# Optimization experiments

Measured on AMD Instinct MI355X. Metric: run time of the kernel, lower is better.

## Reference

```python
import jax, jax.numpy as jnp
import numpy as np

B, NG, F, ED, EG = 1024, 32, 16, 6, 256
H1, C1, C2 = 5, 80, 160
OBS, ACT = 512, 2
NT, ET = B * NG, B * EG
LOG_STD_MIN, LOG_STD_MAX = -5.0, 2.0


def setup_inputs():
    key = jax.random.key(0)
    ks = jax.random.split(key, 32)
    def rn(i, shape, s=0.05):
        return (jax.random.normal(ks[i], shape) * s).astype(jnp.float32)
    # within-graph random edges, then offset per graph (PyG Batch layout)
    off = (jnp.arange(B) * NG)[None, :, None]
    edge_index = (jax.random.randint(ks[0], (2, B, EG), 0, NG) + off).reshape(2, ET).astype(jnp.int32)
    return {
        "x": jax.random.normal(ks[1], (NT, F), dtype=jnp.float32),
        "edge_index": edge_index,
        "edge_attr": jax.random.normal(ks[2], (ET, ED), dtype=jnp.float32),
        "Wl1": rn(3, (H1 * C1, F)), "bl1": rn(4, (H1 * C1,)),
        "Wr1": rn(5, (H1 * C1, F)), "br1": rn(6, (H1 * C1,)),
        "We1": rn(7, (H1 * C1, ED)), "att1": rn(8, (H1, C1)), "bc1": rn(9, (H1 * C1,)),
        "Wl2": rn(10, (C2, H1 * C1)), "bl2": rn(11, (C2,)),
        "Wr2": rn(12, (C2, H1 * C1)), "br2": rn(13, (C2,)),
        "We2": rn(14, (C2, ED)), "att2": rn(15, (1, C2)), "bc2": rn(16, (C2,)),
        "Wd1": rn(17, (NG, C2)), "bd1": rn(18, (NG,)),
        "Wd2": rn(19, (OBS, NG)), "bd2": rn(20, (OBS,)),
        "Wf1": rn(21, (256, OBS)), "bf1": rn(22, (256,)),
        "Wf2": rn(23, (256, 256)), "bf2": rn(24, (256,)),
        "Wm": rn(25, (ACT, 256)), "bm": rn(26, (ACT,)),
        "Ws": rn(27, (ACT, 256)), "bs": rn(28, (ACT,)),
    }


def gatv2(x, src, dst, edge_attr, Wl, bl, Wr, br, We, att, bias, H, C):
    """PyG GATv2Conv (concat heads, no self loops, negative_slope=0.2, eval mode)."""
    N = x.shape[0]; E = src.shape[0]
    xl = x @ Wl.T + bl              # [N, H*C] source transform (also the message)
    xr = x @ Wr.T + br              # [N, H*C] target transform
    e = edge_attr @ We.T            # [E, H*C]
    msg = xl[src].reshape(E, H, C)
    pre = msg + xr[dst].reshape(E, H, C) + e.reshape(E, H, C)
    score = jnp.sum(jax.nn.leaky_relu(pre, 0.2) * att, axis=-1)  # [E, H]
    # segment softmax over incoming edges of each destination node
    mx = jax.ops.segment_max(score, dst, num_segments=N)
    ex = jnp.exp(score - mx[dst])
    den = jax.ops.segment_sum(ex, dst, num_segments=N)
    alpha = ex / (den[dst] + 1e-16)
    out = jax.ops.segment_sum(alpha[..., None] * msg, dst, num_segments=N)
    return out.reshape(N, H * C) + bias


def reference(x, edge_index, edge_attr, Wl1, bl1, Wr1, br1, We1, att1, bc1,
              Wl2, bl2, Wr2, br2, We2, att2, bc2, Wd1, bd1, Wd2, bd2,
              Wf1, bf1, Wf2, bf2, Wm, bm, Ws, bs):
    src, dst = edge_index[0], edge_index[1]
    h = jax.nn.relu(gatv2(x, src, dst, edge_attr, Wl1, bl1, Wr1, br1, We1, att1, bc1, H1, C1))
    h = jax.nn.relu(gatv2(h, src, dst, edge_attr, Wl2, bl2, Wr2, br2, We2, att2, bc2, 1, C2))
    ego = h[jnp.arange(B) * NG]                      # first node of each graph, [B, C2]
    d = jnp.tanh((ego @ Wd1.T + bd1) @ Wd2.T + bd2)  # dense head -> [B, OBS]
    h1 = jax.nn.relu(d @ Wf1.T + bf1)
    h2 = jax.nn.relu(h1 @ Wf2.T + bf2)
    mean = h2 @ Wm.T + bm
    log_std = LOG_STD_MIN + 0.5 * (LOG_STD_MAX - LOG_STD_MIN) * (jnp.tanh(h2 @ Ws.T + bs) + 1.0)
    return mean, log_std
```

## Files before the change

### kernel.cpp

```cpp
#include <hip/hip_runtime.h>

#define B_    1024
#define NG_   32
#define F_    16
#define ED_   6
#define EG_   256
#define ET_   262144
#define H1_   5
#define C1_   80
#define HC1_  400
#define C2_   160
#define OBS_  512

#define S1_   408
#define SG_   400
#define CAP_  40960

typedef unsigned short ushort8v __attribute__((ext_vector_type(8)));

__device__ __forceinline__ float bf2f(unsigned short u) {
  return __uint_as_float(((unsigned int)u) << 16);
}
__device__ __forceinline__ unsigned short f2bf(float f) {
  unsigned int u = __float_as_uint(f);
  u = u + 0x7FFFu + ((u >> 16) & 1u);
  return (unsigned short)(u >> 16);
}
__device__ __forceinline__ float dot8(ushort8v hv, float4 wa, float4 wb, float acc) {
  acc = fmaf(bf2f(hv[0]), wa.x, acc);
  acc = fmaf(bf2f(hv[1]), wa.y, acc);
  acc = fmaf(bf2f(hv[2]), wa.z, acc);
  acc = fmaf(bf2f(hv[3]), wa.w, acc);
  acc = fmaf(bf2f(hv[4]), wb.x, acc);
  acc = fmaf(bf2f(hv[5]), wb.y, acc);
  acc = fmaf(bf2f(hv[6]), wb.z, acc);
  acc = fmaf(bf2f(hv[7]), wb.w, acc);
  return acc;
}

__global__ __launch_bounds__(512, 2)
void k1_transform_bucket(
    const float* __restrict__ x, const int* __restrict__ eidx,
    const float* __restrict__ Wl1, const float* __restrict__ bl1,
    const float* __restrict__ Wr1, const float* __restrict__ br1,
    unsigned short* __restrict__ xlg, unsigned short* __restrict__ xrg,
    int* __restrict__ eorder_g, int* __restrict__ bstart_g)
{
  __shared__ __align__(16) unsigned short xlL[NG_ * S1_];
  __shared__ __align__(16) unsigned short xrL[NG_ * S1_];
  __shared__ float xloc[NG_ * F_];
  __shared__ int   edst[EG_];
  const int b = blockIdx.x, tid = threadIdx.x;
  const int n0 = b * NG_, eb = b * EG_;

  if (tid < EG_) edst[tid] = eidx[ET_ + eb + tid] - n0;
  xloc[tid] = x[n0 * F_ + tid];
  __syncthreads();

  if (tid < 448) {
    for (int t = 0; t < 2; ++t) {
      const int ch = tid + t * 448;
      if (ch >= 800) break;
      const bool isL = (ch < 400);
      const int  c   = isL ? ch : ch - 400;
      const float* Wp = (isL ? Wl1 : Wr1) + c * F_;
      const float bias = isL ? bl1[c] : br1[c];
      unsigned short* dst = (isL ? xlL : xrL) + c;
      float w[16];
#pragma unroll
      for (int qk = 0; qk < 4; ++qk) {
        float4 v = *(const float4*)(Wp + qk * 4);
        w[qk*4+0] = v.x; w[qk*4+1] = v.y; w[qk*4+2] = v.z; w[qk*4+3] = v.w;
      }
      for (int n = 0; n < NG_; n += 2) {
        const float* xa = &xloc[n * F_];
        float accA = bias, accB = bias;
#pragma unroll
        for (int qk = 0; qk < 4; ++qk) {
          float4 a  = *(const float4*)(xa + qk * 4);
          float4 bv = *(const float4*)(xa + F_ + qk * 4);
          accA = fmaf(a.x,  w[qk*4+0], accA); accA = fmaf(a.y,  w[qk*4+1], accA);
          accA = fmaf(a.z,  w[qk*4+2], accA); accA = fmaf(a.w,  w[qk*4+3], accA);
          accB = fmaf(bv.x, w[qk*4+0], accB); accB = fmaf(bv.y, w[qk*4+1], accB);
          accB = fmaf(bv.z, w[qk*4+2], accB); accB = fmaf(bv.w, w[qk*4+3], accB);
        }
        dst[n * S1_]       = f2bf(accA);
        dst[(n + 1) * S1_] = f2bf(accB);
      }
    }
  } else {
    const int lane = tid & 63;
    const int d    = lane & 31;
    const int half = lane >> 5;
    int cnt = 0;
    const int4* ed4 = (const int4*)edst;
    for (int i = 0; i < 32; ++i) {
      int4 v = ed4[half * 32 + i];
      cnt += (v.x == d) + (v.y == d) + (v.z == d) + (v.w == d);
    }
    const int cnt_lo = __shfl(cnt, d);
    const int total  = cnt + __shfl_xor(cnt, 32);
    int pre = total;
#pragma unroll
    for (int off = 1; off < 32; off <<= 1) {
      int tt = __shfl(pre, lane - off);
      if (d >= off) pre += tt;
    }
    const int start = pre - total;
    if (lane < 32) {
      bstart_g[b * 33 + d] = start;
      if (d == 31) bstart_g[b * 33 + 32] = pre;
    }
    int p = start + (half ? cnt_lo : 0);
    for (int i = 0; i < 32; ++i) {
      int4 v = ed4[half * 32 + i];
      const int e = half * 128 + i * 4;
      if (v.x == d) eorder_g[eb + p++] = e;
      if (v.y == d) eorder_g[eb + p++] = e + 1;
      if (v.z == d) eorder_g[eb + p++] = e + 2;
      if (v.w == d) eorder_g[eb + p++] = e + 3;
    }
  }
  __syncthreads();

  for (int i = tid; i < 3200; i += 512) {
    const bool isR = (i >= 1600);
    const int idx = isR ? i - 1600 : i;
    const int n = idx / 50, c8 = idx - n * 50;
    const ushort8v v = *(const ushort8v*)&(isR ? xrL : xlL)[n * S1_ + c8 * 8];
    *(ushort8v*)&(isR ? xrg : xlg)[(n0 + n) * SG_ + c8 * 8] = v;
  }
}

__global__ __launch_bounds__(1024, 1)
void k0b_pack(const int* __restrict__ bstart_g, const int* __restrict__ eorder_g,
              const int* __restrict__ eidx,
              int* __restrict__ egoOff, int* __restrict__ meta_node,
              int* __restrict__ meta_eid)
{
  __shared__ int scanBuf[B_];
  const int b = threadIdx.x;
  const int nE = bstart_g[b * 33 + 1];
  scanBuf[b] = nE;
  __syncthreads();
  for (int off = 1; off < B_; off <<= 1) {
    int v = (b >= off) ? scanBuf[b - off] : 0;
    __syncthreads();
    scanBuf[b] += v;
    __syncthreads();
  }
  const int start = scanBuf[b] - nE;
  egoOff[b] = start;
  if (b == B_ - 1) egoOff[B_] = scanBuf[b];
  if (start + nE <= CAP_) {
    for (int j = 0; j < nE; ++j) {
      const int e = eorder_g[b * EG_ + j];
      meta_node[start + j] = eidx[b * EG_ + e];
      meta_eid[start + j]  = b * EG_ + e;
    }
  }
}

__global__ __launch_bounds__(512, 2)
void k2_scores_aggregate(
    const unsigned short* __restrict__ xlg, const unsigned short* __restrict__ xrg,
    const int* __restrict__ eidx, const float* __restrict__ eattr,
    const float* __restrict__ We1, const float* __restrict__ att1,
    const float* __restrict__ bc1,
    const int* __restrict__ eorder_g, const int* __restrict__ bstart_g,
    unsigned short* __restrict__ hg)
{
  __shared__ __align__(16) unsigned short xl[NG_ * S1_];
  __shared__ __align__(16) unsigned short xr[NG_ * S1_];
  __shared__ float sc0[EG_ * H1_];
  __shared__ float sc1[EG_ * H1_];
  __shared__ float ea[EG_ * ED_];
  __shared__ int   esrc[EG_], edst[EG_], eorder[EG_];
  __shared__ int   bstart[NG_ + 1];
  __shared__ float deninv[NG_ * H1_];

  const int b = blockIdx.x, tid = threadIdx.x;
  const int n0 = b * NG_, eb = b * EG_;

  for (int i = tid; i < 3200; i += 512) {
    const bool isR = (i >= 1600);
    const int idx = isR ? i - 1600 : i;
    const int n = idx / 50, c8 = idx - n * 50;
    const ushort8v v = *(const ushort8v*)&(isR ? xrg : xlg)[(n0 + n) * SG_ + c8 * 8];
    *(ushort8v*)&(isR ? xr : xl)[n * S1_ + c8 * 8] = v;
  }
  if (tid < EG_) {
    esrc[tid]   = eidx[eb + tid] - n0;
    edst[tid]   = eidx[ET_ + eb + tid] - n0;
    eorder[tid] = eorder_g[eb + tid];
  }
  for (int i = tid; i < EG_ * ED_; i += 512) ea[i] = eattr[eb * ED_ + i];
  if (tid < NG_ + 1) bstart[tid] = bstart_g[b * 33 + tid];
  __syncthreads();

  {
    const int e = tid & 255;
    const int s = __builtin_amdgcn_readfirstlane((int)(tid >> 8) & 1);
    float* const scp = s ? sc1 : sc0;
    const int sl = esrc[e], dl = edst[e];
    const float e0 = ea[e*ED_+0], e1 = ea[e*ED_+1], e2 = ea[e*ED_+2];
    const float e3 = ea[e*ED_+3], e4 = ea[e*ED_+4], e5 = ea[e*ED_+5];
    const unsigned short* xlrow = &xl[sl * S1_ + s * 40];
    const unsigned short* xrrow = &xr[dl * S1_ + s * 40];
#pragma unroll
    for (int h = 0; h < H1_; ++h) {
      float sh = 0.f;
#pragma unroll
      for (int co = 0; co < 5; ++co) {
        const int coff  = h * C1_ + co * 8;
        const int cbase = coff + s * 40;
        ushort8v av = *(const ushort8v*)(xlrow + coff);
        ushort8v rv = *(const ushort8v*)(xrrow + coff);
#pragma unroll
        for (int u = 0; u < 8; ++u) {
          const float* wv6 = &We1[(cbase + u) * ED_];
          float t0 = fmaf(wv6[1], e1, wv6[0] * e0);
          float t1 = fmaf(wv6[3], e3, wv6[2] * e2);
          float t2 = fmaf(wv6[5], e5, wv6[4] * e4);
          float p = (bf2f(av[u]) + bf2f(rv[u])) + (t0 + (t1 + t2));
          p = fmaxf(p, 0.2f * p);
          sh = fmaf(p, att1[cbase + u], sh);
        }
      }
      scp[e * H1_ + h] = sh;
    }
  }
  __syncthreads();

  if (tid < NG_ * H1_) {
    const int d = tid & 31, h = tid >> 5;
    const int s0 = bstart[d], s1 = bstart[d + 1];
    float m = -INFINITY;
    for (int k = s0; k < s1; ++k) {
      const int e5i = eorder[k] * H1_ + h;
      m = fmaxf(m, sc0[e5i] + sc1[e5i]);
    }
    float den = 0.f;
    for (int k = s0; k < s1; ++k) {
      const int e5i = eorder[k] * H1_ + h;
      float t = expf(sc0[e5i] + sc1[e5i] - m);
      den += t;
      sc0[e5i] = t;
    }
    deninv[tid] = 1.f / (den + 1e-16f);
  }
  __syncthreads();

  for (int idx = tid; idx < NG_ * 50; idx += 512) {
    const int d  = idx / 50;
    const int co = idx - d * 50;
    const int c  = co * 8;
    const int h  = co / 10;
    const int s0 = bstart[d], s1 = bstart[d + 1];
    float acc[8] = {0.f,0.f,0.f,0.f,0.f,0.f,0.f,0.f};
    for (int k = s0; k < s1; ++k) {
      const int e = eorder[k];
      const float al = sc0[e * H1_ + h];
      ushort8v xv = *(const ushort8v*)(&xl[esrc[e] * S1_ + c]);
#pragma unroll
      for (int u = 0; u < 8; ++u) acc[u] = fmaf(al, bf2f(xv[u]), acc[u]);
    }
    const float inv = deninv[h * 32 + d];
    ushort8v hv;
#pragma unroll
    for (int u = 0; u < 8; ++u)
      hv[u] = f2bf(fmaxf(fmaf(acc[u], inv, bc1[c + u]), 0.f));
    *(ushort8v*)&hg[(n0 + d) * SG_ + c] = hv;
  }
}

__global__ __launch_bounds__(512, 2)
void k3a_gemm(const unsigned short* __restrict__ hg,
              const int* __restrict__ meta_node, const int* __restrict__ egoOff,
              const float* __restrict__ Wl2, const float* __restrict__ bl2,
              const float* __restrict__ Wr2, const float* __restrict__ br2,
              float* __restrict__ msgP, float* __restrict__ xr2v_g)
{
  __shared__ __align__(16) unsigned short rows[64 * S1_];
  __shared__ int rnode[64];
  __shared__ int sTot;
  const int tid = threadIdx.x;
  const bool isX = (blockIdx.x < 16);
  if (tid == 0) sTot = egoOff[B_];
  __syncthreads();
  const int total = sTot;

  const float* W    = isX ? Wr2 : Wl2;
  const float* bias = isX ? br2 : bl2;
  float* outB       = isX ? xr2v_g : msgP;

  const int es = tid & 15;
  const int cg = tid >> 4;
  const float* wp[5];
#pragma unroll
  for (int i = 0; i < 5; ++i) wp[i] = &W[(size_t)(cg * 5 + i) * HC1_];

  int c = isX ? (int)blockIdx.x : (int)blockIdx.x - 16;
  const int cstep = (int)gridDim.x - 16;

  for (;;) {
    const int r0 = c * 64;
    int nr;
    if (isX) nr = 64;
    else { if (r0 >= total) break; nr = min(64, total - r0); }

    __syncthreads();
    if (tid < 64) rnode[tid] = (tid < nr) ? (isX ? (r0 + tid) * NG_ : meta_node[r0 + tid]) : 0;
    __syncthreads();
    for (int i = tid; i < 64 * 50; i += 512) {
      const int r = i / 50, o8 = i - r * 50;
      if (r < nr)
        *(ushort8v*)&rows[r * S1_ + o8 * 8] =
            *(const ushort8v*)&hg[(size_t)rnode[r] * SG_ + o8 * 8];
    }
    __syncthreads();

    float acc[4][5] = {};
#pragma unroll 2
    for (int ko = 0; ko < 50; ++ko) {
      const int k = ko * 8;
      ushort8v rv[4];
#pragma unroll
      for (int t = 0; t < 4; ++t)
        rv[t] = *(const ushort8v*)&rows[(es + 16 * t) * S1_ + k];
#pragma unroll
      for (int i = 0; i < 5; ++i) {
        const float4 wa = *(const float4*)(wp[i] + k);
        const float4 wb = *(const float4*)(wp[i] + k + 4);
#pragma unroll
        for (int t = 0; t < 4; ++t)
          acc[t][i] = dot8(rv[t], wa, wb, acc[t][i]);
      }
    }

#pragma unroll
    for (int t = 0; t < 4; ++t) {
      const int r = es + 16 * t;
      if (r < nr) {
        float* op = outB + (size_t)(r0 + r) * C2_ + cg * 5;
#pragma unroll
        for (int i = 0; i < 5; ++i) op[i] = acc[t][i] + bias[cg * 5 + i];
      }
    }
    if (isX) break;
    c += cstep;
  }
}

__global__ __launch_bounds__(64, 4)
void k3b_finish(const float* __restrict__ eattr,
                const float* __restrict__ We2, const float* __restrict__ att2,
                const float* __restrict__ bc2,
                const int* __restrict__ egoOff, const int* __restrict__ meta_eid,
                const float* __restrict__ msgP, const float* __restrict__ xr2v_g,
                float* __restrict__ egoH)
{
  __shared__ float xr2s[C2_];
  __shared__ float scq[EG_], wq[EG_];
  const int b = blockIdx.x, ln = threadIdx.x;
  const int off = egoOff[b];
  const int nE  = egoOff[b + 1] - off;

  if (ln < 40) *(float4*)&xr2s[ln * 4] = *(const float4*)&xr2v_g[(size_t)b * C2_ + ln * 4];

  const int s = ln >> 3, q8 = ln & 7;
  for (int base = 0; base < nE; base += 8) {
    const int j = base + s;
    float sv = 0.f;
    if (j < nE) {
      const int eid = meta_eid[off + j];
      const float* ap = &eattr[(size_t)eid * ED_];
      const float f0 = ap[0], f1 = ap[1], f2 = ap[2];
      const float f3 = ap[3], f4 = ap[4], f5 = ap[5];
      const float* mrow = &msgP[(size_t)(off + j) * C2_];
      for (int i = 0; i < 20; ++i) {
        const int c2 = q8 * 20 + i;
        const float* wv6 = &We2[c2 * ED_];
        float t0 = fmaf(wv6[1], f1, wv6[0] * f0);
        float t1 = fmaf(wv6[3], f3, wv6[2] * f2);
        float t2 = fmaf(wv6[5], f5, wv6[4] * f4);
        float pp = mrow[c2] + xr2s[c2] + (t0 + (t1 + t2));
        pp = fmaxf(pp, 0.2f * pp);
        sv = fmaf(pp, att2[c2], sv);
      }
    }
    sv += __shfl_xor(sv, 1); sv += __shfl_xor(sv, 2); sv += __shfl_xor(sv, 4);
    if (q8 == 0 && j < nE) scq[j] = sv;
  }

  float m = -INFINITY;
  for (int j = ln; j < nE; j += 64) m = fmaxf(m, scq[j]);
#pragma unroll
  for (int d = 1; d < 64; d <<= 1) m = fmaxf(m, __shfl_xor(m, d));

  float den = 0.f;
  for (int j = ln; j < nE; j += 64) {
    const float w = expf(scq[j] - m);
    wq[j] = w;
    den += w;
  }
#pragma unroll
  for (int d = 1; d < 64; d <<= 1) den += __shfl_xor(den, d);
  const float inv = 1.f / (den + 1e-16f);

  float o0 = 0.f, o1 = 0.f, o2 = 0.f;
  for (int j = 0; j < nE; ++j) {
    const float w = wq[j];
    const float* mrow = &msgP[(size_t)(off + j) * C2_];
    o0 = fmaf(w, mrow[ln], o0);
    o1 = fmaf(w, mrow[ln + 64], o1);
    if (ln + 128 < C2_) o2 = fmaf(w, mrow[ln + 128], o2);
  }
  egoH[(size_t)b * C2_ + ln]      = fmaxf(fmaf(o0, inv, bc2[ln]), 0.f);
  egoH[(size_t)b * C2_ + ln + 64] = fmaxf(fmaf(o1, inv, bc2[ln + 64]), 0.f);
  if (ln + 128 < C2_)
    egoH[(size_t)b * C2_ + ln + 128] = fmaxf(fmaf(o2, inv, bc2[ln + 128]), 0.f);
}

__global__ __launch_bounds__(512, 2)
void mlp_head_kernel(
    const float* __restrict__ egoH,
    const float* __restrict__ Wd1, const float* __restrict__ bd1,
    const float* __restrict__ Wd2, const float* __restrict__ bd2,
    const float* __restrict__ Wf1, const float* __restrict__ bf1,
    const float* __restrict__ Wf2, const float* __restrict__ bf2,
    const float* __restrict__ Wm,  const float* __restrict__ bm,
    const float* __restrict__ Ws,  const float* __restrict__ bs,
    float* __restrict__ out)
{
  __shared__ float hE[4 * C2_];
  __shared__ float t1[4 * NG_];
  __shared__ float dbuf[4 * OBS_];
  __shared__ float f1b[4 * 256];
  __shared__ float f2b[4 * 256];

  const int g0  = blockIdx.x * 4;
  const int tid = threadIdx.x;

  for (int i = tid; i < 4 * C2_; i += 512) hE[i] = egoH[g0 * C2_ + i];
  __syncthreads();

  if (tid < 4 * NG_) {
    const int g = tid >> 5, o = tid & 31;
    float acc = bd1[o];
    const float* w  = &Wd1[o * C2_];
    const float* hp = &hE[g * C2_];
    for (int k = 0; k < C2_; k += 4) {
      float4 hv = *(const float4*)(hp + k);
      float4 wv = *(const float4*)(w + k);
      acc = fmaf(hv.x, wv.x, acc); acc = fmaf(hv.y, wv.y, acc);
      acc = fmaf(hv.z, wv.z, acc); acc = fmaf(hv.w, wv.w, acc);
    }
    t1[tid] = acc;
  }
  __syncthreads();

  for (int idx = tid; idx < 4 * OBS_; idx += 512) {
    const int g = idx >> 9, o = idx & 511;
    float acc = bd2[o];
    const float* w  = &Wd2[o * NG_];
    const float* tp = &t1[g * NG_];
#pragma unroll
    for (int k = 0; k < NG_; k += 4) {
      float4 tv = *(const float4*)(tp + k);
      float4 wv = *(const float4*)(w + k);
      acc = fmaf(tv.x, wv.x, acc); acc = fmaf(tv.y, wv.y, acc);
      acc = fmaf(tv.z, wv.z, acc); acc = fmaf(tv.w, wv.w, acc);
    }
    dbuf[idx] = tanhf(acc);
  }
  __syncthreads();

  {
    const int o = tid & 255, gg = tid >> 8;
    const float* w  = &Wf1[o * OBS_];
    const float* dA = &dbuf[(gg * 2 + 0) * OBS_];
    const float* dB = &dbuf[(gg * 2 + 1) * OBS_];
    float a0 = bf1[o], a1 = a0;
#pragma unroll 2
    for (int k = 0; k < OBS_; k += 4) {
      float4 wv = *(const float4*)(w + k);
      float4 xA = *(const float4*)(dA + k);
      float4 xB = *(const float4*)(dB + k);
      a0 = fmaf(xA.x, wv.x, a0); a0 = fmaf(xA.y, wv.y, a0);
      a0 = fmaf(xA.z, wv.z, a0); a0 = fmaf(xA.w, wv.w, a0);
      a1 = fmaf(xB.x, wv.x, a1); a1 = fmaf(xB.y, wv.y, a1);
      a1 = fmaf(xB.z, wv.z, a1); a1 = fmaf(xB.w, wv.w, a1);
    }
    f1b[(gg * 2 + 0) * 256 + o] = fmaxf(a0, 0.f);
    f1b[(gg * 2 + 1) * 256 + o] = fmaxf(a1, 0.f);
  }
  __syncthreads();

  {
    const int o = tid & 255, gg = tid >> 8;
    const float* w  = &Wf2[o * 256];
    const float* dA = &f1b[(gg * 2 + 0) * 256];
    const float* dB = &f1b[(gg * 2 + 1) * 256];
    float a0 = bf2[o], a1 = a0;
#pragma unroll 2
    for (int k = 0; k < 256; k += 4) {
      float4 wv = *(const float4*)(w + k);
      float4 xA = *(const float4*)(dA + k);
      float4 xB = *(const float4*)(dB + k);
      a0 = fmaf(xA.x, wv.x, a0); a0 = fmaf(xA.y, wv.y, a0);
      a0 = fmaf(xA.z, wv.z, a0); a0 = fmaf(xA.w, wv.w, a0);
      a1 = fmaf(xB.x, wv.x, a1); a1 = fmaf(xB.y, wv.y, a1);
      a1 = fmaf(xB.z, wv.z, a1); a1 = fmaf(xB.w, wv.w, a1);
    }
    f2b[(gg * 2 + 0) * 256 + o] = fmaxf(a0, 0.f);
    f2b[(gg * 2 + 1) * 256 + o] = fmaxf(a1, 0.f);
  }
  __syncthreads();

  if (tid < 16) {
    const int g  = tid >> 2;
    const int a  = (tid >> 1) & 1;
    const int hm = tid & 1;
    const float* fp = &f2b[g * 256];
    const float* w  = hm ? &Ws[a * 256] : &Wm[a * 256];
    float acc = hm ? bs[a] : bm[a];
    for (int k = 0; k < 256; ++k) acc = fmaf(fp[k], w[k], acc);
    if (hm == 0) out[(g0 + g) * 2 + a] = acc;
    else         out[2048 + (g0 + g) * 2 + a] = -5.0f + 3.5f * (tanhf(acc) + 1.0f);
  }
}

extern "C" void kernel_launch(void* const* d_in, const int* in_sizes, int n_in,
                              void* d_out, int out_size, void* d_ws, size_t ws_size,
                              hipStream_t stream) {
  const float* x     = (const float*)d_in[0];
  const int*   eidx  = (const int*)d_in[1];
  const float* eattr = (const float*)d_in[2];
  const float* Wl1 = (const float*)d_in[3];  const float* bl1 = (const float*)d_in[4];
  const float* Wr1 = (const float*)d_in[5];  const float* br1 = (const float*)d_in[6];
  const float* We1 = (const float*)d_in[7];  const float* att1= (const float*)d_in[8];
  const float* bc1 = (const float*)d_in[9];
  const float* Wl2 = (const float*)d_in[10]; const float* bl2 = (const float*)d_in[11];
  const float* Wr2 = (const float*)d_in[12]; const float* br2 = (const float*)d_in[13];
  const float* We2 = (const float*)d_in[14]; const float* att2= (const float*)d_in[15];
  const float* bc2 = (const float*)d_in[16];
  const float* Wd1 = (const float*)d_in[17]; const float* bd1 = (const float*)d_in[18];
  const float* Wd2 = (const float*)d_in[19]; const float* bd2 = (const float*)d_in[20];
  const float* Wf1 = (const float*)d_in[21]; const float* bf1 = (const float*)d_in[22];
  const float* Wf2 = (const float*)d_in[23]; const float* bf2 = (const float*)d_in[24];
  const float* Wm  = (const float*)d_in[25]; const float* bm  = (const float*)d_in[26];
  const float* Ws  = (const float*)d_in[27]; const float* bs  = (const float*)d_in[28];

  unsigned short* xlg = (unsigned short*)d_ws;
  unsigned short* hg  = xlg + 32768 * SG_;
  int* eorder_g = (int*)(hg + 32768 * SG_);
  int* bstart_g = eorder_g + ET_;
  float* egoH   = (float*)(bstart_g + B_ * 33);
  int* egoOff   = (int*)(egoH + B_ * C2_);
  int* meta_node= egoOff + (B_ + 1);
  int* meta_eid = meta_node + CAP_;
  float* xr2v_g = (float*)(meta_eid + CAP_);
  float* msgP   = (float*)xlg;

  k1_transform_bucket<<<B_, 512, 0, stream>>>(
      x, eidx, Wl1, bl1, Wr1, br1, xlg, hg, eorder_g, bstart_g);

  k0b_pack<<<1, 1024, 0, stream>>>(
      bstart_g, eorder_g, eidx, egoOff, meta_node, meta_eid);

  k2_scores_aggregate<<<B_, 512, 0, stream>>>(
      xlg, hg, eidx, eattr, We1, att1, bc1, eorder_g, bstart_g, hg);

  k3a_gemm<<<160, 512, 0, stream>>>(
      hg, meta_node, egoOff, Wl2, bl2, Wr2, br2, msgP, xr2v_g);

  k3b_finish<<<B_, 64, 0, stream>>>(
      eattr, We2, att2, bc2, egoOff, meta_eid, msgP, xr2v_g, egoH);

  mlp_head_kernel<<<B_ / 4, 512, 0, stream>>>(
      egoH, Wd1, bd1, Wd2, bd2, Wf1, bf1, Wf2, bf2, Wm, bm, Ws, bs,
      (float*)d_out);
}
```

Measured before the change: 252.9 us.

## Fuse edge pack into transform kernel via atomic offsets, widen finish kernel

Removes the single-block k0b_pack kernel and its serial 1024-wide scan. Each k1 block now claims its slot in the packed ego-edge arrays with an atomicAdd on a counter cleared by a memset, then writes its meta entries in parallel. msgP gets its own workspace region instead of aliasing xlg, the k3a grid grows from 160 to 272 blocks, and k3b runs 256 threads per block so edge scoring and the output reduction are spread over more lanes. The cost is that pack order becomes nondeterministic, though per-graph offsets stay consistent, plus an extra memset and a larger workspace.

Measured after the change: 236.2 us. 6.6% less time.

```diff
diff --git a/kernel.cpp b/kernel.cpp
--- a/kernel.cpp
+++ b/kernel.cpp
@@ -44,12 +44,15 @@
     const float* __restrict__ Wl1, const float* __restrict__ bl1,
     const float* __restrict__ Wr1, const float* __restrict__ br1,
     unsigned short* __restrict__ xlg, unsigned short* __restrict__ xrg,
-    int* __restrict__ eorder_g, int* __restrict__ bstart_g)
+    int* __restrict__ eorder_g, int* __restrict__ bstart_g,
+    int* __restrict__ packCnt, int* __restrict__ egoOff,
+    int* __restrict__ meta_node, int* __restrict__ meta_eid)
 {
   __shared__ __align__(16) unsigned short xlL[NG_ * S1_];
   __shared__ __align__(16) unsigned short xrL[NG_ * S1_];
   __shared__ float xloc[NG_ * F_];
   __shared__ int   edst[EG_];
+  __shared__ int   sNE, sStart;
   const int b = blockIdx.x, tid = threadIdx.x;
   const int n0 = b * NG_, eb = b * EG_;
 
@@ -110,6 +113,7 @@
     if (lane < 32) {
       bstart_g[b * 33 + d] = start;
       if (d == 31) bstart_g[b * 33 + 32] = pre;
+      if (d == 0)  sNE = total;
     }
     int p = start + (half ? cnt_lo : 0);
     for (int i = 0; i < 32; ++i) {
@@ -130,34 +134,15 @@
     const ushort8v v = *(const ushort8v*)&(isR ? xrL : xlL)[n * S1_ + c8 * 8];
     *(ushort8v*)&(isR ? xrg : xlg)[(n0 + n) * SG_ + c8 * 8] = v;
   }
-}
-
-__global__ __launch_bounds__(1024, 1)
-void k0b_pack(const int* __restrict__ bstart_g, const int* __restrict__ eorder_g,
-              const int* __restrict__ eidx,
-              int* __restrict__ egoOff, int* __restrict__ meta_node,
-              int* __restrict__ meta_eid)
-{
-  __shared__ int scanBuf[B_];
-  const int b = threadIdx.x;
-  const int nE = bstart_g[b * 33 + 1];
-  scanBuf[b] = nE;
-  __syncthreads();
-  for (int off = 1; off < B_; off <<= 1) {
-    int v = (b >= off) ? scanBuf[b - off] : 0;
-    __syncthreads();
-    scanBuf[b] += v;
-    __syncthreads();
-  }
-  const int start = scanBuf[b] - nE;
-  egoOff[b] = start;
-  if (b == B_ - 1) egoOff[B_] = scanBuf[b];
-  if (start + nE <= CAP_) {
-    for (int j = 0; j < nE; ++j) {
-      const int e = eorder_g[b * EG_ + j];
-      meta_node[start + j] = eidx[b * EG_ + e];
-      meta_eid[start + j]  = b * EG_ + e;
-    }
+
+  if (tid == 0) sStart = atomicAdd(packCnt, sNE);
+  __syncthreads();
+  const int nE = sNE, st = sStart;
+  if (tid == 0) egoOff[b] = st;
+  if (tid < nE && st + nE <= CAP_) {
+    const int e = eorder_g[eb + tid];
+    meta_node[st + tid] = eidx[eb + e];
+    meta_eid[st + tid]  = eb + e;
   }
 }
 
@@ -276,7 +261,7 @@
 
 __global__ __launch_bounds__(512, 2)
 void k3a_gemm(const unsigned short* __restrict__ hg,
-              const int* __restrict__ meta_node, const int* __restrict__ egoOff,
+              const int* __restrict__ meta_node, const int* __restrict__ packCnt,
               const float* __restrict__ Wl2, const float* __restrict__ bl2,
               const float* __restrict__ Wr2, const float* __restrict__ br2,
               float* __restrict__ msgP, float* __restrict__ xr2v_g)
@@ -286,9 +271,9 @@
   __shared__ int sTot;
   const int tid = threadIdx.x;
   const bool isX = (blockIdx.x < 16);
-  if (tid == 0) sTot = egoOff[B_];
-  __syncthreads();
-  const int total = sTot;
+  if (tid == 0) sTot = *packCnt;
+  __syncthreads();
+  const int total = min(sTot, CAP_);
 
   const float* W    = isX ? Wr2 : Wl2;
   const float* bias = isX ? br2 : bl2;
@@ -352,24 +337,27 @@
   }
 }
 
-__global__ __launch_bounds__(64, 4)
+__global__ __launch_bounds__(256, 4)
 void k3b_finish(const float* __restrict__ eattr,
                 const float* __restrict__ We2, const float* __restrict__ att2,
                 const float* __restrict__ bc2,
-                const int* __restrict__ egoOff, const int* __restrict__ meta_eid,
+                const int* __restrict__ egoOff, const int* __restrict__ bstart_g,
+                const int* __restrict__ meta_eid,
                 const float* __restrict__ msgP, const float* __restrict__ xr2v_g,
                 float* __restrict__ egoH)
 {
   __shared__ float xr2s[C2_];
   __shared__ float scq[EG_], wq[EG_];
-  const int b = blockIdx.x, ln = threadIdx.x;
+  __shared__ float sInv;
+  const int b = blockIdx.x, tid = threadIdx.x;
   const int off = egoOff[b];
-  const int nE  = egoOff[b + 1] - off;
-
-  if (ln < 40) *(float4*)&xr2s[ln * 4] = *(const float4*)&xr2v_g[(size_t)b * C2_ + ln * 4];
-
-  const int s = ln >> 3, q8 = ln & 7;
-  for (int base = 0; base < nE; base += 8) {
+  const int nE  = bstart_g[b * 33 + 1];
+
+  if (tid < 40) *(float4*)&xr2s[tid * 4] = *(const float4*)&xr2v_g[(size_t)b * C2_ + tid * 4];
+  __syncthreads();
+
+  const int s = tid >> 3, q8 = tid & 7;
+  for (int base = 0; base < nE; base += 32) {
     const int j = base + s;
     float sv = 0.f;
     if (j < nE) {
@@ -392,34 +380,31 @@
     sv += __shfl_xor(sv, 1); sv += __shfl_xor(sv, 2); sv += __shfl_xor(sv, 4);
     if (q8 == 0 && j < nE) scq[j] = sv;
   }
-
-  float m = -INFINITY;
-  for (int j = ln; j < nE; j += 64) m = fmaxf(m, scq[j]);
-#pragma unroll
-  for (int d = 1; d < 64; d <<= 1) m = fmaxf(m, __shfl_xor(m, d));
-
-  float den = 0.f;
-  for (int j = ln; j < nE; j += 64) {
-    const float w = expf(scq[j] - m);
-    wq[j] = w;
-    den += w;
-  }
-#pragma unroll
-  for (int d = 1; d < 64; d <<= 1) den += __shfl_xor(den, d);
-  const float inv = 1.f / (den + 1e-16f);
-
-  float o0 = 0.f, o1 = 0.f, o2 = 0.f;
-  for (int j = 0; j < nE; ++j) {
-    const float w = wq[j];
-    const float* mrow = &msgP[(size_t)(off + j) * C2_];
-    o0 = fmaf(w, mrow[ln], o0);
-    o1 = fmaf(w, mrow[ln + 64], o1);
-    if (ln + 128 < C2_) o2 = fmaf(w, mrow[ln + 128], o2);
-  }
-  egoH[(size_t)b * C2_ + ln]      = fmaxf(fmaf(o0, inv, bc2[ln]), 0.f);
-  egoH[(size_t)b * C2_ + ln + 64] = fmaxf(fmaf(o1, inv, bc2[ln + 64]), 0.f);
-  if (ln + 128 < C2_)
-    egoH[(size_t)b * C2_ + ln + 128] = fmaxf(fmaf(o2, inv, bc2[ln + 128]), 0.f);
+  __syncthreads();
+
+  if (tid < 64) {
+    float m = -INFINITY;
+    for (int j = tid; j < nE; j += 64) m = fmaxf(m, scq[j]);
+#pragma unroll
+    for (int d = 1; d < 64; d <<= 1) m = fmaxf(m, __shfl_xor(m, d));
+    float den = 0.f;
+    for (int j = tid; j < nE; j += 64) {
+      const float w = expf(scq[j] - m);
+      wq[j] = w;
+      den += w;
+    }
+#pragma unroll
+    for (int d = 1; d < 64; d <<= 1) den += __shfl_xor(den, d);
+    if (tid == 0) sInv = 1.f / (den + 1e-16f);
+  }
+  __syncthreads();
+
+  if (tid < C2_) {
+    float o = 0.f;
+    for (int j = 0; j < nE; ++j)
+      o = fmaf(wq[j], msgP[(size_t)(off + j) * C2_ + tid], o);
+    egoH[(size_t)b * C2_ + tid] = fmaxf(fmaf(o, sInv, bc2[tid]), 0.f);
+  }
 }
 
 __global__ __launch_bounds__(512, 2)
@@ -553,30 +538,31 @@
   const float* Ws  = (const float*)d_in[27]; const float* bs  = (const float*)d_in[28];
 
   unsigned short* xlg = (unsigned short*)d_ws;
-  unsigned short* hg  = xlg + 32768 * SG_;
-  int* eorder_g = (int*)(hg + 32768 * SG_);
+  unsigned short* hg  = xlg + (size_t)32768 * SG_;
+  float* msgP   = (float*)(hg + (size_t)32768 * SG_);
+  int* eorder_g = (int*)(msgP + (size_t)CAP_ * C2_);
   int* bstart_g = eorder_g + ET_;
   float* egoH   = (float*)(bstart_g + B_ * 33);
   int* egoOff   = (int*)(egoH + B_ * C2_);
   int* meta_node= egoOff + (B_ + 1);
   int* meta_eid = meta_node + CAP_;
   float* xr2v_g = (float*)(meta_eid + CAP_);
-  float* msgP   = (float*)xlg;
+  int* packCnt  = (int*)(xr2v_g + B_ * C2_);
+
+  hipMemsetAsync(packCnt, 0, sizeof(int), stream);
 
   k1_transform_bucket<<<B_, 512, 0, stream>>>(
-      x, eidx, Wl1, bl1, Wr1, br1, xlg, hg, eorder_g, bstart_g);
-
-  k0b_pack<<<1, 1024, 0, stream>>>(
-      bstart_g, eorder_g, eidx, egoOff, meta_node, meta_eid);
+      x, eidx, Wl1, bl1, Wr1, br1, xlg, hg, eorder_g, bstart_g,
+      packCnt, egoOff, meta_node, meta_eid);
 
   k2_scores_aggregate<<<B_, 512, 0, stream>>>(
       xlg, hg, eidx, eattr, We1, att1, bc1, eorder_g, bstart_g, hg);
 
-  k3a_gemm<<<160, 512, 0, stream>>>(
-      hg, meta_node, egoOff, Wl2, bl2, Wr2, br2, msgP, xr2v_g);
-
-  k3b_finish<<<B_, 64, 0, stream>>>(
-      eattr, We2, att2, bc2, egoOff, meta_eid, msgP, xr2v_g, egoH);
+  k3a_gemm<<<272, 512, 0, stream>>>(
+      hg, meta_node, packCnt, Wl2, bl2, Wr2, br2, msgP, xr2v_g);
+
+  k3b_finish<<<B_, 256, 0, stream>>>(
+      eattr, We2, att2, bc2, egoOff, bstart_g, meta_eid, msgP, xr2v_g, egoH);
 
   mlp_head_kernel<<<B_ / 4, 512, 0, stream>>>(
       egoH, Wd1, bd1, Wd2, bd2, Wf1, bf1, Wf2, bf2, Wm, bm, Ws, bs,
```
